# Optimization experiments

Hardware: AMD Instinct MI355X
Metric: run time of the kernel (lower is better)

Reference implementation:

```python
import jax, jax.numpy as jnp
import numpy as np

EMBED_DIM = 1024
NUM_HEADS = 16
HEAD_DIM = EMBED_DIM // NUM_HEADS
B, N = 4, 2048


def setup_inputs() -> dict:
    key = jax.random.key(0)
    ks = jax.random.split(key, 12)
    s = 1.0 / np.sqrt(EMBED_DIM)
    inp = {
        "x": jax.random.normal(ks[0], (B, N, EMBED_DIM), dtype=jnp.float32),
        "dist_matrix": jax.random.uniform(ks[1], (N, N), dtype=jnp.float32),
        # Linear weights stored torch-style [out, in]
        "Wq": jax.random.normal(ks[2], (EMBED_DIM, EMBED_DIM), dtype=jnp.float32) * s,
        "bq": jnp.zeros((EMBED_DIM,), dtype=jnp.float32),
        "Wk": jax.random.normal(ks[3], (EMBED_DIM, EMBED_DIM), dtype=jnp.float32) * s,
        "bk": jnp.zeros((EMBED_DIM,), dtype=jnp.float32),
        "Wv": jax.random.normal(ks[4], (EMBED_DIM, EMBED_DIM), dtype=jnp.float32) * s,
        "bv": jnp.zeros((EMBED_DIM,), dtype=jnp.float32),
        "Wo": jax.random.normal(ks[5], (EMBED_DIM, EMBED_DIM), dtype=jnp.float32) * s,
        "bo": jnp.zeros((EMBED_DIM,), dtype=jnp.float32),
        # DistanceBias params: bias = dist_w * dist + dist_b (learned scalar affine)
        "dist_w": jnp.asarray(-1.0, dtype=jnp.float32),
        "dist_b": jnp.asarray(0.0, dtype=jnp.float32),
    }
    return inp


def reference(x, dist_matrix, Wq, bq, Wk, bk, Wv, bv, Wo, bo, dist_w, dist_b):
    b, n, c = x.shape
    h, d = NUM_HEADS, HEAD_DIM
    # projections (torch Linear: x @ W.T + b), reshape to [b, h, n, d]
    def proj(W, bias):
        y = jnp.einsum('bnc,oc->bno', x, W) + bias
        return y.reshape(b, n, h, d).transpose(0, 2, 1, 3)
    q = proj(Wq, bq)
    k = proj(Wk, bk)
    v = proj(Wv, bv)
    scores = jnp.einsum('bhnd,bhmd->bhnm', q, k) / np.sqrt(d).astype(np.float32)
    bias = dist_w * dist_matrix + dist_b            # [N, N], shared over b, h
    scores = scores + bias[None, None, :, :]
    attn = jax.nn.softmax(scores, axis=-1)
    out = jnp.einsum('bhnm,bhmd->bhnd', attn, v)    # [b, h, n, d]
    out = out.transpose(0, 2, 1, 3).reshape(b, n, c)
    return jnp.einsum('bnc,oc->bno', out, Wo) + bo
```

## Files before the change

kernel.cpp:

```cpp
#include <hip/hip_runtime.h>
#include <stdint.h>

typedef unsigned short ushort;
typedef __attribute__((ext_vector_type(8))) short bf16x8;
typedef __attribute__((ext_vector_type(4))) float f32x4;
typedef __attribute__((ext_vector_type(16))) float f32x16;

__device__ __forceinline__ float b2f(ushort u) {
    return __uint_as_float(((unsigned)u) << 16);
}
__device__ __forceinline__ ushort f2b(float f) {
    unsigned u = __float_as_uint(f);
    u += 0x7fff + ((u >> 16) & 1);
    return (ushort)(u >> 16);
}

#if __has_builtin(__builtin_amdgcn_exp2f)
#define EXP2(x) __builtin_amdgcn_exp2f(x)
#else
#define EXP2(x) __expf((x) * 0.69314718056f)
#endif

__device__ __forceinline__ unsigned cvtpk(float a, float b) {
    unsigned r;
    asm("v_cvt_pk_bf16_f32 %0, %1, %2" : "=v"(r) : "v"(a), "v"(b));
    return r;
}

__device__ __forceinline__ void plswap(unsigned &a, unsigned &b) {
#if __has_builtin(__builtin_amdgcn_permlane32_swap)
    auto r = __builtin_amdgcn_permlane32_swap(a, b, 0, 0);
    a = (unsigned)r[0]; b = (unsigned)r[1];
#else
    asm volatile("v_permlane32_swap_b32 %0, %1" : "+v"(a), "+v"(b));
#endif
}

#define SEQN 2048
#define EMB  1024
#define NH   16
#define HD   64
#define BHSTRIDE (SEQN * HD)

__device__ __forceinline__ void gload16(const ushort* g, ushort* l) {
    __builtin_amdgcn_global_load_lds(
        (const __attribute__((address_space(1))) unsigned int*)g,
        (__attribute__((address_space(3))) unsigned int*)l, 16, 0, 0);
}

__global__ __launch_bounds__(256) void conv_x(
        const float* __restrict__ s, ushort* __restrict__ d) {
    const size_t i = (size_t)blockIdx.x * 256 + threadIdx.x;
    float4 a = ((const float4*)s)[2 * i];
    float4 b = ((const float4*)s)[2 * i + 1];
    ushort pk[8] = {f2b(a.x), f2b(a.y), f2b(a.z), f2b(a.w),
                    f2b(b.x), f2b(b.y), f2b(b.z), f2b(b.w)};
    ((uint4*)d)[i] = *(uint4*)pk;
}

__global__ __launch_bounds__(256) void conv_w4(
        const float* __restrict__ W0, const float* __restrict__ W1,
        const float* __restrict__ W2, const float* __restrict__ W3,
        ushort* __restrict__ d) {
    const float* s = (blockIdx.y == 0) ? W0 : (blockIdx.y == 1) ? W1
                   : (blockIdx.y == 2) ? W2 : W3;
    ushort* dst = d + ((size_t)blockIdx.y << 20);
    const size_t i = (size_t)blockIdx.x * 256 + threadIdx.x;
    float4 a = ((const float4*)s)[2 * i];
    float4 b = ((const float4*)s)[2 * i + 1];
    ushort pk[8] = {f2b(a.x), f2b(a.y), f2b(a.z), f2b(a.w),
                    f2b(b.x), f2b(b.y), f2b(b.z), f2b(b.w)};
    ((uint4*)dst)[i] = *(uint4*)pk;
}

__global__ __launch_bounds__(256) void conv_Lp(
        const float* __restrict__ dist, const float* __restrict__ dw,
        const float* __restrict__ db, float* __restrict__ Lp) {
    const float c1 = dw[0] * 1.44269504f, c2 = db[0] * 1.44269504f;
    const size_t gid = (size_t)blockIdx.x * 256 + threadIdx.x;
    const int lo  = (int)(gid & 31);
    const int kv4 = (int)((gid >> 5) & 511);
    const int qt  = (int)(gid >> 14);
    const int q   = qt * 32 + lo;
    float4 d = *(const float4*)(dist + (size_t)q * SEQN + kv4 * 4);
    float4 o = {fmaf(d.x, c1, c2), fmaf(d.y, c1, c2),
                fmaf(d.z, c1, c2), fmaf(d.w, c1, c2)};
    ((float4*)Lp)[gid] = o;
}

#define LDSZ (128 * 32)

__global__ __launch_bounds__(256) void gemm_qkv(
        const ushort* __restrict__ xb, const ushort* __restrict__ Wb,
        const float* __restrict__ bq, const float* __restrict__ bk,
        const float* __restrict__ bv,
        ushort* __restrict__ qb, ushort* __restrict__ kb,
        ushort* __restrict__ vT) {
    __shared__ ushort As[2][LDSZ];
    __shared__ ushort Bs[2][LDSZ];
    const int m0   = blockIdx.x * 128;
    const int nt   = blockIdx.y;
    const int wsel = nt >> 3;
    const int n0   = (nt & 7) * 128;
    const ushort* W    = Wb + ((size_t)wsel << 20);
    const float* bias  = (wsel == 0) ? bq : (wsel == 1) ? bk : bv;

    const int t = threadIdx.x, lane = t & 63, wave = t >> 6;
    const int ln = lane & 15, quad = lane >> 4;
    const int wm = wave & 1, wn = wave >> 1;

    const int e0 = wave * 128 + lane;
    const int e1 = e0 + 64;
    const ushort* gA0 = xb + (size_t)(m0 + (e0 >> 2)) * 1024 + (e0 & 3) * 8;
    const ushort* gA1 = xb + (size_t)(m0 + (e1 >> 2)) * 1024 + (e1 & 3) * 8;
    const ushort* gB0 = W  + (size_t)(n0 + (e0 >> 2)) * 1024 + (e0 & 3) * 8;
    const ushort* gB1 = W  + (size_t)(n0 + (e1 >> 2)) * 1024 + (e1 & 3) * 8;
    ushort* lA0a = &As[0][wave * 1024]; ushort* lA0b = lA0a + 512;
    ushort* lA1a = &As[1][wave * 1024]; ushort* lA1b = lA1a + 512;
    ushort* lB0a = &Bs[0][wave * 1024]; ushort* lB0b = lB0a + 512;
    ushort* lB1a = &Bs[1][wave * 1024]; ushort* lB1b = lB1a + 512;

    f32x4 acc[4][4];
#pragma unroll
    for (int i = 0; i < 4; i++)
#pragma unroll
        for (int j = 0; j < 4; j++) acc[i][j] = (f32x4){0.f, 0.f, 0.f, 0.f};

    for (int k0 = 0; k0 < 1024; k0 += 64) {
        __syncthreads();
        gload16(gA0 + k0,      lA0a); gload16(gA1 + k0,      lA0b);
        gload16(gB0 + k0,      lB0a); gload16(gB1 + k0,      lB0b);
        gload16(gA0 + k0 + 32, lA1a); gload16(gA1 + k0 + 32, lA1b);
        gload16(gB0 + k0 + 32, lB1a); gload16(gB1 + k0 + 32, lB1b);
        __syncthreads();
#pragma unroll
        for (int kk2 = 0; kk2 < 2; kk2++) {
            bf16x8 af[4], bfr[4];
#pragma unroll
            for (int i = 0; i < 4; i++)
                af[i]  = *(bf16x8*)&As[kk2][(wm * 64 + i * 16 + ln) * 32 + quad * 8];
#pragma unroll
            for (int j = 0; j < 4; j++)
                bfr[j] = *(bf16x8*)&Bs[kk2][(wn * 64 + j * 16 + ln) * 32 + quad * 8];
#pragma unroll
            for (int i = 0; i < 4; i++)
#pragma unroll
                for (int j = 0; j < 4; j++)
                    acc[i][j] = __builtin_amdgcn_mfma_f32_16x16x32_bf16(
                                    af[i], bfr[j], acc[i][j], 0, 0, 0);
        }
    }

    if (wsel < 2) {
        ushort* dst = (wsel == 0) ? qb : kb;
        const float scale = (wsel == 0) ? 0.125f : 1.0f;
#pragma unroll
        for (int j = 0; j < 4; j++) {
            const int o  = n0 + wn * 64 + j * 16 + ln;
            const float bval = bias[o];
            const int h = o >> 6, d = o & 63;
#pragma unroll
            for (int i = 0; i < 4; i++) {
                const int mg = m0 + wm * 64 + i * 16 + quad * 4;
#pragma unroll
                for (int r = 0; r < 4; r++) {
                    const int m  = mg + r;
                    const int b  = m >> 11;
                    const int ns = m & 2047;
                    dst[(size_t)(b * NH + h) * BHSTRIDE + (size_t)ns * HD + d] =
                        f2b((acc[i][j][r] + bval) * scale);
                }
            }
        }
    } else {
#pragma unroll
        for (int j = 0; j < 4; j++) {
            const int o  = n0 + wn * 64 + j * 16 + ln;
            const float bval = bias[o];
            const int h = o >> 6, d = o & 63;
#pragma unroll
            for (int i = 0; i < 4; i++) {
                const int mg = m0 + wm * 64 + i * 16 + quad * 4;
                const int b  = mg >> 11;
                const int ns = mg & 2047;
                ushort pk[4];
#pragma unroll
                for (int r = 0; r < 4; r++) pk[r] = f2b(acc[i][j][r] + bval);
                *(uint2*)&vT[(size_t)(b * NH + h) * BHSTRIDE +
                             (size_t)d * SEQN + ns] = *(uint2*)&pk[0];
            }
        }
    }
}

__global__ __launch_bounds__(256, 4) void attn(
        ushort* q,
        const ushort* __restrict__ k,
        const ushort* __restrict__ vT,
        const float* __restrict__ Lp) {
    __shared__ short Ks[2][64 * 72];
    __shared__ short Vs[2][64 * 72];
    const int t = threadIdx.x, lane = t & 63, wave = t >> 6;
    const int lo = lane & 31, hi = lane >> 5;
    const int wid  = blockIdx.x + (blockIdx.y << 4) + (blockIdx.z << 8);
    const int xcd  = wid & 7;
    const int slot = wid >> 3;
    const int bh   = xcd * 8 + (slot >> 4);
    const int qx   = slot & 15;
    const int qw0 = qx * 128 + wave * 32;

    ushort* qp = q + (size_t)bh * BHSTRIDE;
    const ushort* kp = k  + (size_t)bh * BHSTRIDE;
    const ushort* vp = vT + (size_t)bh * BHSTRIDE;
    const float4* Lp4 = (const float4*)Lp + ((size_t)(qw0 >> 5) * 512) * 32 + lo;

    const int sr = t >> 2;
    const int sc = (t & 3) * 16;

    bf16x8 qf[4];
#pragma unroll
    for (int kk = 0; kk < 4; kk++)
        qf[kk] = *(const bf16x8*)(qp + (size_t)(qw0 + lo) * HD + kk * 16 + hi * 8);

    f32x16 O[2];
#pragma unroll
    for (int dt = 0; dt < 2; dt++)
#pragma unroll
        for (int i = 0; i < 16; i++) O[dt][i] = 0.f;
    float lsum = 0.f;

    uint4 krg0 = *(const uint4*)(kp + (size_t)sr * HD + sc);
    uint4 krg1 = *(const uint4*)(kp + (size_t)sr * HD + sc + 8);
    uint4 vrg0 = *(const uint4*)(vp + (size_t)sr * SEQN + sc);
    uint4 vrg1 = *(const uint4*)(vp + (size_t)sr * SEQN + sc + 8);
    *(uint4*)&Ks[0][sr * 72 + sc]     = krg0;
    *(uint4*)&Ks[0][sr * 72 + sc + 8] = krg1;
    *(uint4*)&Vs[0][sr * 72 + sc]     = vrg0;
    *(uint4*)&Vs[0][sr * 72 + sc + 8] = vrg1;
    krg0 = *(const uint4*)(kp + (size_t)(64 + sr) * HD + sc);
    krg1 = *(const uint4*)(kp + (size_t)(64 + sr) * HD + sc + 8);
    vrg0 = *(const uint4*)(vp + (size_t)sr * SEQN + 64 + sc);
    vrg1 = *(const uint4*)(vp + (size_t)sr * SEQN + 64 + sc + 8);

    for (int kt = 0; kt < 32; kt++) {
        const int kv0 = kt * 64;
        const int cb = kt & 1;
        __syncthreads();
        *(uint4*)&Ks[cb ^ 1][sr * 72 + sc]     = krg0;
        *(uint4*)&Ks[cb ^ 1][sr * 72 + sc + 8] = krg1;
        *(uint4*)&Vs[cb ^ 1][sr * 72 + sc]     = vrg0;
        *(uint4*)&Vs[cb ^ 1][sr * 72 + sc + 8] = vrg1;
        const int kvn = (kv0 + 128) & 2047;
        krg0 = *(const uint4*)(kp + (size_t)(kvn + sr) * HD + sc);
        krg1 = *(const uint4*)(kp + (size_t)(kvn + sr) * HD + sc + 8);
        vrg0 = *(const uint4*)(vp + (size_t)sr * SEQN + kvn + sc);
        vrg1 = *(const uint4*)(vp + (size_t)sr * SEQN + kvn + sc + 8);
        float4 lv2[2][4];
#pragma unroll
        for (int s = 0; s < 2; s++)
#pragma unroll
            for (int n = 0; n < 4; n++)
                lv2[s][n] = Lp4[((kv0 >> 2) + s * 8 + hi + 2 * n) * 32];

#pragma unroll
        for (int s = 0; s < 2; s++) {
            f32x16 z;
#pragma unroll
            for (int i = 0; i < 16; i++) z[i] = 0.f;
            __builtin_amdgcn_s_setprio(1);
#pragma unroll
            for (int kk = 0; kk < 4; kk++) {
                bf16x8 kf = *(bf16x8*)&Ks[cb][(s * 32 + lo) * 72 + kk * 16 + hi * 8];
                z = __builtin_amdgcn_mfma_f32_32x32x16_bf16(kf, qf[kk], z, 0, 0, 0);
            }
            __builtin_amdgcn_s_setprio(0);
            float p[16];
#pragma unroll
            for (int n = 0; n < 4; n++) {
#pragma unroll
                for (int m = 0; m < 4; m++) {
                    float pv = EXP2(fmaf(z[n * 4 + m], 1.44269504f,
                                         ((const float*)&lv2[s][n])[m]));
                    lsum += pv;
                    p[n * 4 + m] = pv;
                }
            }
#pragma unroll
            for (int kl = 0; kl < 2; kl++) {
                unsigned a0 = cvtpk(p[kl * 8 + 0], p[kl * 8 + 1]);
                unsigned b0 = cvtpk(p[kl * 8 + 4], p[kl * 8 + 5]);
                plswap(a0, b0);
                unsigned a1 = cvtpk(p[kl * 8 + 2], p[kl * 8 + 3]);
                unsigned b1 = cvtpk(p[kl * 8 + 6], p[kl * 8 + 7]);
                plswap(a1, b1);
                union { bf16x8 v; unsigned u[4]; } pf;
                pf.u[0] = a0; pf.u[1] = a1; pf.u[2] = b0; pf.u[3] = b1;
                const int kvk = s * 2 + kl;
                __builtin_amdgcn_s_setprio(1);
#pragma unroll
                for (int dt = 0; dt < 2; dt++) {
                    bf16x8 vf = *(bf16x8*)&Vs[cb][(dt * 32 + lo) * 72 +
                                                  kvk * 16 + hi * 8];
                    O[dt] = __builtin_amdgcn_mfma_f32_32x32x16_bf16(
                                vf, pf.v, O[dt], 0, 0, 0);
                }
                __builtin_amdgcn_s_setprio(0);
            }
        }
    }

    float tot = lsum + __shfl_xor(lsum, 32);
    const float inv = 1.0f / tot;
#pragma unroll
    for (int dt = 0; dt < 2; dt++)
#pragma unroll
        for (int n = 0; n < 4; n++) {
            uint2 pk2;
            pk2.x = cvtpk(O[dt][n * 4 + 0] * inv, O[dt][n * 4 + 1] * inv);
            pk2.y = cvtpk(O[dt][n * 4 + 2] * inv, O[dt][n * 4 + 3] * inv);
            *(uint2*)(qp + (size_t)(qw0 + lo) * HD + dt * 32 + hi * 4 + n * 8)
                = pk2;
        }
}

__global__ __launch_bounds__(256) void gemm_out(
        const ushort* __restrict__ ao, const ushort* __restrict__ Wob,
        const float* __restrict__ bias, float* __restrict__ out) {
    __shared__ ushort As[2][LDSZ];
    __shared__ ushort Bs[2][LDSZ];
    const int m0 = blockIdx.x * 128;
    const int n0 = blockIdx.y * 128;
    const int t = threadIdx.x, lane = t & 63, wave = t >> 6;
    const int ln = lane & 15, quad = lane >> 4;
    const int wm = wave & 1, wn = wave >> 1;

    const int e0 = wave * 128 + lane;
    const int e1 = e0 + 64;
    const int bb = m0 >> 11;
    const int nbase = m0 & 2047;
    const ushort* gA0 = ao + ((size_t)bb << 21) +
                        (size_t)(nbase + (e0 >> 2)) * 64 + (e0 & 3) * 8;
    const ushort* gA1 = ao + ((size_t)bb << 21) +
                        (size_t)(nbase + (e1 >> 2)) * 64 + (e1 & 3) * 8;
    const ushort* gB0 = Wob + (size_t)(n0 + (e0 >> 2)) * 1024 + (e0 & 3) * 8;
    const ushort* gB1 = Wob + (size_t)(n0 + (e1 >> 2)) * 1024 + (e1 & 3) * 8;
    ushort* lA0a = &As[0][wave * 1024]; ushort* lA0b = lA0a + 512;
    ushort* lA1a = &As[1][wave * 1024]; ushort* lA1b = lA1a + 512;
    ushort* lB0a = &Bs[0][wave * 1024]; ushort* lB0b = lB0a + 512;
    ushort* lB1a = &Bs[1][wave * 1024]; ushort* lB1b = lB1a + 512;

    f32x4 acc[4][4];
#pragma unroll
    for (int i = 0; i < 4; i++)
#pragma unroll
        for (int j = 0; j < 4; j++) acc[i][j] = (f32x4){0.f, 0.f, 0.f, 0.f};

    for (int k0 = 0; k0 < 1024; k0 += 64) {
        const size_t aoff = ((size_t)(k0 >> 6) << 17);
        __syncthreads();
        gload16(gA0 + aoff,      lA0a); gload16(gA1 + aoff,      lA0b);
        gload16(gB0 + k0,        lB0a); gload16(gB1 + k0,        lB0b);
        gload16(gA0 + aoff + 32, lA1a); gload16(gA1 + aoff + 32, lA1b);
        gload16(gB0 + k0 + 32,   lB1a); gload16(gB1 + k0 + 32,   lB1b);
        __syncthreads();
#pragma unroll
        for (int kk2 = 0; kk2 < 2; kk2++) {
            bf16x8 af[4], bfr[4];
#pragma unroll
            for (int i = 0; i < 4; i++)
                af[i]  = *(bf16x8*)&As[kk2][(wm * 64 + i * 16 + ln) * 32 + quad * 8];
#pragma unroll
            for (int j = 0; j < 4; j++)
                bfr[j] = *(bf16x8*)&Bs[kk2][(wn * 64 + j * 16 + ln) * 32 + quad * 8];
#pragma unroll
            for (int i = 0; i < 4; i++)
#pragma unroll
                for (int j = 0; j < 4; j++)
                    acc[i][j] = __builtin_amdgcn_mfma_f32_16x16x32_bf16(
                                    af[i], bfr[j], acc[i][j], 0, 0, 0);
        }
    }

#pragma unroll
    for (int j = 0; j < 4; j++) {
        const int o = n0 + wn * 64 + j * 16 + ln;
        const float bval = bias[o];
#pragma unroll
        for (int i = 0; i < 4; i++) {
            const int mg = m0 + wm * 64 + i * 16 + quad * 4;
#pragma unroll
            for (int r = 0; r < 4; r++)
                out[(size_t)(mg + r) * EMB + o] = acc[i][j][r] + bval;
        }
    }
}

extern "C" void kernel_launch(void* const* d_in, const int* in_sizes, int n_in,
                              void* d_out, int out_size, void* d_ws, size_t ws_size,
                              hipStream_t stream) {
    const float* x    = (const float*)d_in[0];
    const float* dist = (const float*)d_in[1];
    const float* Wq   = (const float*)d_in[2];
    const float* bq   = (const float*)d_in[3];
    const float* Wk   = (const float*)d_in[4];
    const float* bk   = (const float*)d_in[5];
    const float* Wv   = (const float*)d_in[6];
    const float* bv   = (const float*)d_in[7];
    const float* Wo   = (const float*)d_in[8];
    const float* bo   = (const float*)d_in[9];
    const float* dw   = (const float*)d_in[10];
    const float* db   = (const float*)d_in[11];

    const size_t PLANE = (size_t)8192 * 1024;
    ushort* qb = (ushort*)d_ws;
    ushort* kb = qb + PLANE;
    ushort* xb = kb + PLANE;
    ushort* Wb = xb + PLANE;
    ushort* vT = (ushort*)d_out;
    float*  Lf = (float*)(vT + PLANE);

    dim3 blk(256);
    conv_x       <<<dim3(4096),      blk, 0, stream>>>(x, xb);
    conv_w4      <<<dim3(512, 4),    blk, 0, stream>>>(Wq, Wk, Wv, Wo, Wb);
    conv_Lp      <<<dim3(4096),      blk, 0, stream>>>(dist, dw, db, Lf);
    gemm_qkv     <<<dim3(64, 24),    blk, 0, stream>>>(xb, Wb, bq, bk, bv,
                                                       qb, kb, vT);
    attn         <<<dim3(16, 16, 4), blk, 0, stream>>>(qb, kb, vT, Lf);
    gemm_out     <<<dim3(64, 8),     blk, 0, stream>>>(qb, Wb + 3 * (size_t)(1 << 20),
                                                       bo, (float*)d_out);
}
```

Baseline: 315.3 us.

## Restructure attention loop to interleave LDS stores and prefetches between sub-tiles

Splits each 64-key tile into two explicitly written 32-key halves. The shared-memory stores of the next tile and the bias prefetch now sit between the halves, and the global K/V prefetch moves to the end of the iteration. The bias loads are double-buffered across iterations. The block-to-(batch,head) mapping also drops the XCD-aware swizzle and uses the plain grid indices, which changes L2 locality across dies. The intent is to hide memory latency behind MFMA work, at the cost of more live registers and losing K/V sharing within each XCD.

Measured after the change: 340.9 us. 8.1% more time.

```diff
diff --git a/kernel.cpp b/kernel.cpp
--- a/kernel.cpp
+++ b/kernel.cpp
@@ -202,12 +202,9 @@
     __shared__ short Vs[2][64 * 72];
     const int t = threadIdx.x, lane = t & 63, wave = t >> 6;
     const int lo = lane & 31, hi = lane >> 5;
-    const int wid  = blockIdx.x + (blockIdx.y << 4) + (blockIdx.z << 8);
-    const int xcd  = wid & 7;
-    const int slot = wid >> 3;
-    const int bh   = xcd * 8 + (slot >> 4);
-    const int qx   = slot & 15;
-    const int qw0 = qx * 128 + wave * 32;
+    const int h = blockIdx.y, b = blockIdx.z;
+    const int bh = b * NH + h;
+    const int qw0 = blockIdx.x * 128 + wave * 32;
 
     ushort* qp = q + (size_t)bh * BHSTRIDE;
     const ushort* kp = k  + (size_t)bh * BHSTRIDE;
@@ -241,50 +238,42 @@
     krg1 = *(const uint4*)(kp + (size_t)(64 + sr) * HD + sc + 8);
     vrg0 = *(const uint4*)(vp + (size_t)sr * SEQN + 64 + sc);
     vrg1 = *(const uint4*)(vp + (size_t)sr * SEQN + 64 + sc + 8);
-
+    float4 lv0[2][4];
+#pragma unroll
+    for (int n = 0; n < 4; n++)
+        lv0[0][n] = Lp4[(hi + 2 * n) * 32];
+
+#pragma unroll 2
     for (int kt = 0; kt < 32; kt++) {
         const int kv0 = kt * 64;
         const int cb = kt & 1;
         __syncthreads();
-        *(uint4*)&Ks[cb ^ 1][sr * 72 + sc]     = krg0;
-        *(uint4*)&Ks[cb ^ 1][sr * 72 + sc + 8] = krg1;
-        *(uint4*)&Vs[cb ^ 1][sr * 72 + sc]     = vrg0;
-        *(uint4*)&Vs[cb ^ 1][sr * 72 + sc + 8] = vrg1;
-        const int kvn = (kv0 + 128) & 2047;
-        krg0 = *(const uint4*)(kp + (size_t)(kvn + sr) * HD + sc);
-        krg1 = *(const uint4*)(kp + (size_t)(kvn + sr) * HD + sc + 8);
-        vrg0 = *(const uint4*)(vp + (size_t)sr * SEQN + kvn + sc);
-        vrg1 = *(const uint4*)(vp + (size_t)sr * SEQN + kvn + sc + 8);
-        float4 lv2[2][4];
-#pragma unroll
-        for (int s = 0; s < 2; s++)
-#pragma unroll
-            for (int n = 0; n < 4; n++)
-                lv2[s][n] = Lp4[((kv0 >> 2) + s * 8 + hi + 2 * n) * 32];
-
-#pragma unroll
-        for (int s = 0; s < 2; s++) {
+        float4 lv1[4];
+#pragma unroll
+        for (int n = 0; n < 4; n++)
+            lv1[n] = Lp4[((kv0 >> 2) + 8 + hi + 2 * n) * 32];
+
+        {
             f32x16 z;
 #pragma unroll
             for (int i = 0; i < 16; i++) z[i] = 0.f;
             __builtin_amdgcn_s_setprio(1);
 #pragma unroll
             for (int kk = 0; kk < 4; kk++) {
-                bf16x8 kf = *(bf16x8*)&Ks[cb][(s * 32 + lo) * 72 + kk * 16 + hi * 8];
+                bf16x8 kf = *(bf16x8*)&Ks[cb][lo * 72 + kk * 16 + hi * 8];
                 z = __builtin_amdgcn_mfma_f32_32x32x16_bf16(kf, qf[kk], z, 0, 0, 0);
             }
             __builtin_amdgcn_s_setprio(0);
             float p[16];
 #pragma unroll
-            for (int n = 0; n < 4; n++) {
+            for (int n = 0; n < 4; n++)
 #pragma unroll
                 for (int m = 0; m < 4; m++) {
                     float pv = EXP2(fmaf(z[n * 4 + m], 1.44269504f,
-                                         ((const float*)&lv2[s][n])[m]));
+                                         ((const float*)&lv0[cb][n])[m]));
                     lsum += pv;
                     p[n * 4 + m] = pv;
                 }
-            }
 #pragma unroll
             for (int kl = 0; kl < 2; kl++) {
                 unsigned a0 = cvtpk(p[kl * 8 + 0], p[kl * 8 + 1]);
@@ -295,7 +284,61 @@
                 plswap(a1, b1);
                 union { bf16x8 v; unsigned u[4]; } pf;
                 pf.u[0] = a0; pf.u[1] = a1; pf.u[2] = b0; pf.u[3] = b1;
-                const int kvk = s * 2 + kl;
+                __builtin_amdgcn_s_setprio(1);
+#pragma unroll
+                for (int dt = 0; dt < 2; dt++) {
+                    bf16x8 vf = *(bf16x8*)&Vs[cb][(dt * 32 + lo) * 72 +
+                                                  kl * 16 + hi * 8];
+                    O[dt] = __builtin_amdgcn_mfma_f32_32x32x16_bf16(
+                                vf, pf.v, O[dt], 0, 0, 0);
+                }
+                __builtin_amdgcn_s_setprio(0);
+            }
+        }
+
+        *(uint4*)&Ks[cb ^ 1][sr * 72 + sc]     = krg0;
+        *(uint4*)&Ks[cb ^ 1][sr * 72 + sc + 8] = krg1;
+        *(uint4*)&Vs[cb ^ 1][sr * 72 + sc]     = vrg0;
+        *(uint4*)&Vs[cb ^ 1][sr * 72 + sc + 8] = vrg1;
+        {
+            const int kv0n = (kv0 + 64) & 2047;
+#pragma unroll
+            for (int n = 0; n < 4; n++)
+                lv0[cb ^ 1][n] = Lp4[((kv0n >> 2) + hi + 2 * n) * 32];
+        }
+
+        {
+            f32x16 z;
+#pragma unroll
+            for (int i = 0; i < 16; i++) z[i] = 0.f;
+            __builtin_amdgcn_s_setprio(1);
+#pragma unroll
+            for (int kk = 0; kk < 4; kk++) {
+                bf16x8 kf = *(bf16x8*)&Ks[cb][(32 + lo) * 72 + kk * 16 + hi * 8];
+                z = __builtin_amdgcn_mfma_f32_32x32x16_bf16(kf, qf[kk], z, 0, 0, 0);
+            }
+            __builtin_amdgcn_s_setprio(0);
+            float p[16];
+#pragma unroll
+            for (int n = 0; n < 4; n++)
+#pragma unroll
+                for (int m = 0; m < 4; m++) {
+                    float pv = EXP2(fmaf(z[n * 4 + m], 1.44269504f,
+                                         ((const float*)&lv1[n])[m]));
+                    lsum += pv;
+                    p[n * 4 + m] = pv;
+                }
+#pragma unroll
+            for (int kl = 0; kl < 2; kl++) {
+                unsigned a0 = cvtpk(p[kl * 8 + 0], p[kl * 8 + 1]);
+                unsigned b0 = cvtpk(p[kl * 8 + 4], p[kl * 8 + 5]);
+                plswap(a0, b0);
+                unsigned a1 = cvtpk(p[kl * 8 + 2], p[kl * 8 + 3]);
+                unsigned b1 = cvtpk(p[kl * 8 + 6], p[kl * 8 + 7]);
+                plswap(a1, b1);
+                union { bf16x8 v; unsigned u[4]; } pf;
+                pf.u[0] = a0; pf.u[1] = a1; pf.u[2] = b0; pf.u[3] = b1;
+                const int kvk = 2 + kl;
                 __builtin_amdgcn_s_setprio(1);
 #pragma unroll
                 for (int dt = 0; dt < 2; dt++) {
@@ -306,6 +349,14 @@
                 }
                 __builtin_amdgcn_s_setprio(0);
             }
+        }
+
+        {
+            const int kvn = (kv0 + 128) & 2047;
+            krg0 = *(const uint4*)(kp + (size_t)(kvn + sr) * HD + sc);
+            krg1 = *(const uint4*)(kp + (size_t)(kvn + sr) * HD + sc + 8);
+            vrg0 = *(const uint4*)(vp + (size_t)sr * SEQN + kvn + sc);
+            vrg1 = *(const uint4*)(vp + (size_t)sr * SEQN + kvn + sc + 8);
         }
     }
 
```
